# Optimization experiments

Measured on AMD Instinct MI355X. Metric: run time of the kernel, lower is better.

The kernel has to match this reference:

```python
import jax, jax.numpy as jnp
import numpy as np

H = 128          # hidden_dim
L = 3            # n_layers
G = 128          # num graphs in batch
BN_EPS = 1e-5


def setup_inputs() -> dict:
    key = jax.random.key(0)
    ks = jax.random.split(key, 16)
    N, E, ND, ED = 2048, 8192, 32, 16
    s = lambda k, shape, fan: jax.random.normal(k, shape, dtype=jnp.float32) / np.sqrt(fan)
    return {
        "x": jax.random.normal(ks[0], (N, ND), dtype=jnp.float32),
        "edge_index": jax.random.randint(ks[1], (2, E), 0, N),
        "edge_attr": jax.random.normal(ks[2], (E, ED), dtype=jnp.float32),
        "batch": jnp.sort(jax.random.randint(ks[3], (N,), 0, G)),
        "node_W": s(ks[4], (ND, H), ND),
        "node_b": jnp.zeros((H,), jnp.float32),
        "edge_W": s(ks[5], (L, ED, H * H), ED),
        "edge_b": jnp.zeros((L, H * H), jnp.float32),
        "root_W": s(ks[6], (L, H, H), H),
        "conv_bias": jnp.zeros((L, H), jnp.float32),
        "bn_gamma": jnp.ones((L, H), jnp.float32),
        "bn_beta": jnp.zeros((L, H), jnp.float32),
        "cls_W1": s(ks[7], (H, 64), H),
        "cls_b1": jnp.zeros((64,), jnp.float32),
        "cls_W2": s(ks[8], (64, 1), 64),
        "cls_b2": jnp.zeros((1,), jnp.float32),
    }


def _segment_mean(vals, ids, num_segments):
    ssum = jax.ops.segment_sum(vals, ids, num_segments=num_segments)
    cnt = jax.ops.segment_sum(jnp.ones((vals.shape[0],), vals.dtype), ids,
                              num_segments=num_segments)
    return ssum / jnp.maximum(cnt, 1.0)[:, None]


def reference(x, edge_index, edge_attr, batch, node_W, node_b, edge_W, edge_b,
              root_W, conv_bias, bn_gamma, bn_beta, cls_W1, cls_b1, cls_W2, cls_b2):
    N = x.shape[0]
    src, dst = edge_index[0], edge_index[1]
    h = x @ node_W + node_b                                   # [N, H]
    for l in range(L):
        # edge-conditioned weights: [E, H, H]
        W = (edge_attr @ edge_W[l] + edge_b[l]).reshape(-1, H, H)
        msg = jnp.einsum('ei,eio->eo', h[src], W)             # gather + per-edge matmul
        agg = _segment_mean(msg, dst, N)                      # scatter-mean
        x_new = h @ root_W[l] + agg + conv_bias[l]
        # BatchNorm (batch statistics, training-mode math)
        mu = jnp.mean(x_new, axis=0)
        var = jnp.var(x_new, axis=0)
        x_new = (x_new - mu) * jax.lax.rsqrt(var + BN_EPS) * bn_gamma[l] + bn_beta[l]
        x_new = jax.nn.relu(x_new)                            # dropout omitted (eval)
        h = h + x_new                                         # residual
    g = _segment_mean(h, batch, G)                            # global mean pool [G, H]
    out = jax.nn.relu(g @ cls_W1 + cls_b1) @ cls_W2 + cls_b2  # classifier
    return out.squeeze(-1)                                    # [G]
```

## Files before the change

kernel.cpp:

```cpp
#include <hip/hip_runtime.h>
#include <cstddef>
#include <cstdint>

#define H 128
#define EDIM 16
#define NLAYER 3
#define NSLICE 18
#define WCOLS (NSLICE * H)
#define PCOLS (EDIM * H)
#define TM 64
#define TN 64
#define TK 16

typedef unsigned short ushort_t;
typedef unsigned int uint_t;
typedef __attribute__((ext_vector_type(8))) short bf16x8;
typedef __attribute__((ext_vector_type(4))) float f32x4;

__device__ __forceinline__ ushort_t f2bf(float f) {
    uint_t u = __builtin_bit_cast(uint_t, f);
    u += 0x7fffu + ((u >> 16) & 1u);
    return (ushort_t)(u >> 16);
}
__device__ __forceinline__ float bf_lo(uint_t u) {
    return __builtin_bit_cast(float, u << 16);
}
__device__ __forceinline__ float bf_hi(uint_t u) {
    return __builtin_bit_cast(float, u & 0xffff0000u);
}

__global__ __launch_bounds__(256) void setup_kernel(
    const int* __restrict__ dst, const int* __restrict__ batch,
    int* __restrict__ hist, float* __restrict__ cntG, int E, int N,
    const float* __restrict__ eW, const float* __restrict__ eb,
    const float* __restrict__ rW, ushort_t* __restrict__ Wt)
{
    if (blockIdx.x < 32) {
        int t = blockIdx.x * 256 + threadIdx.x;
        if (t < E) atomicAdd(&hist[dst[t]], 1);
        if (t < N) atomicAdd(&cntG[batch[t]], 1.f);
        return;
    }
    __shared__ ushort_t tile[128][136];
    const int b = blockIdx.x - 32;
    const int l = b / NSLICE, s = b % NSLICE;
    const float* S = (s < 16) ? (eW + ((size_t)l * 16 + s) * (H * H))
                   : (s == 16 ? (eb + (size_t)l * H * H)
                              : (rW + (size_t)l * H * H));
    const int t = threadIdx.x;
    const int k = t >> 1, o0 = (t & 1) * 64;
#pragma unroll
    for (int j = 0; j < 64; j += 4) {
        float4 v = *(const float4*)&S[(size_t)k * H + o0 + j];
        tile[k][o0 + j + 0] = f2bf(v.x);
        tile[k][o0 + j + 1] = f2bf(v.y);
        tile[k][o0 + j + 2] = f2bf(v.z);
        tile[k][o0 + j + 3] = f2bf(v.w);
    }
    __syncthreads();
    const int n = t >> 1, k0 = (t & 1) * 64;
    ushort_t* outp = Wt + ((size_t)l * WCOLS + s * H + n) * H + k0;
#pragma unroll 8
    for (int j = 0; j < 64; ++j) outp[j] = tile[k0 + j][n];
}

__global__ __launch_bounds__(256) void scan_kernel(
    const int* __restrict__ hist, int* __restrict__ offs, int N)
{
    __shared__ int part[256];
    const int t = threadIdx.x;
    const int base = t * 8;
    int v[8], loc[8], s = 0;
#pragma unroll
    for (int j = 0; j < 8; ++j) v[j] = hist[base + j];
#pragma unroll
    for (int j = 0; j < 8; ++j) { loc[j] = s; s += v[j]; }
    part[t] = s;
    __syncthreads();
    for (int off = 1; off < 256; off <<= 1) {
        int x = (t >= off) ? part[t - off] : 0;
        __syncthreads();
        part[t] += x;
        __syncthreads();
    }
    const int boff = (t == 0) ? 0 : part[t - 1];
#pragma unroll
    for (int j = 0; j < 8; ++j) offs[base + j] = boff + loc[j];
    if (t == 255) offs[N] = boff + s;
}

__global__ void scatter_kernel(const int* __restrict__ dst,
                               const int* __restrict__ offs,
                               int* __restrict__ fill, int* __restrict__ eord, int E)
{
    const int e = blockIdx.x * 256 + threadIdx.x;
    if (e >= E) return;
    const int d = dst[e];
    const int pos = offs[d] + atomicAdd(&fill[d], 1);
    eord[pos] = e;
}

__global__ __launch_bounds__(256) void gemm_embed(
    const float* __restrict__ A, const float* __restrict__ B,
    const float* __restrict__ bias, float* __restrict__ C,
    ushort_t* __restrict__ Cbf, int M, int K, int N)
{
    __shared__ float As[TK][TM + 4];
    __shared__ float Bs[TK][TN + 4];
    const int bm = blockIdx.y * TM;
    const int bn = blockIdx.x * TN;
    const int tid = threadIdx.x;
    const int tx = tid & 15;
    const int ty = tid >> 4;

    float acc[4][4];
#pragma unroll
    for (int i = 0; i < 4; ++i)
#pragma unroll
        for (int j = 0; j < 4; ++j) acc[i][j] = 0.f;

    const int ka = tid & 15, ma = tid >> 4;
    const int nb = tid & 63, kb = tid >> 6;

    for (int k0 = 0; k0 < K; k0 += TK) {
#pragma unroll
        for (int r = 0; r < 4; ++r)
            As[ka][ma + 16 * r] = A[(size_t)(bm + ma + 16 * r) * K + (k0 + ka)];
#pragma unroll
        for (int r = 0; r < 4; ++r)
            Bs[kb + 4 * r][nb] = B[(size_t)(k0 + kb + 4 * r) * N + bn + nb];
        __syncthreads();
#pragma unroll
        for (int kk = 0; kk < TK; ++kk) {
            const float4 a4 = *(const float4*)&As[kk][ty * 4];
            const float4 b4 = *(const float4*)&Bs[kk][tx * 4];
            const float a[4] = {a4.x, a4.y, a4.z, a4.w};
            const float b[4] = {b4.x, b4.y, b4.z, b4.w};
#pragma unroll
            for (int i = 0; i < 4; ++i)
#pragma unroll
                for (int j = 0; j < 4; ++j)
                    acc[i][j] = fmaf(a[i], b[j], acc[i][j]);
        }
        __syncthreads();
    }

#pragma unroll
    for (int i = 0; i < 4; ++i) {
        const int row = bm + ty * 4 + i;
        float4 v;
        v.x = acc[i][0] + bias[(bn + tx * 4 + 0) & 127];
        v.y = acc[i][1] + bias[(bn + tx * 4 + 1) & 127];
        v.z = acc[i][2] + bias[(bn + tx * 4 + 2) & 127];
        v.w = acc[i][3] + bias[(bn + tx * 4 + 3) & 127];
        *(float4*)&C[(size_t)row * N + bn + tx * 4] = v;
        ushort_t* o = &Cbf[(size_t)row * N + bn + tx * 4];
        o[0] = f2bf(v.x); o[1] = f2bf(v.y); o[2] = f2bf(v.z); o[3] = f2bf(v.w);
    }
}

__global__ __launch_bounds__(256) void mfma_gemm(
    const ushort_t* __restrict__ hbf, const ushort_t* __restrict__ Wt,
    ushort_t* __restrict__ Pb, float* __restrict__ QR)
{
    __shared__ ushort_t As[64][136];
    __shared__ ushort_t Bs[64][136];
    const int tid = threadIdx.x;
    const int v0 = blockIdx.y * 64;
    const int n0 = blockIdx.x * 64;

    {
        const int row = tid >> 2, col0 = (tid & 3) * 32;
        const ushort_t* ga = hbf + (size_t)(v0 + row) * H + col0;
        const ushort_t* gb = Wt + (size_t)(n0 + row) * H + col0;
#pragma unroll
        for (int j = 0; j < 32; j += 8) {
            *(uint4*)&As[row][col0 + j] = *(const uint4*)(ga + j);
            *(uint4*)&Bs[row][col0 + j] = *(const uint4*)(gb + j);
        }
    }
    __syncthreads();

    const int wave = tid >> 6, lane = tid & 63;
    const int l15 = lane & 15, kg = lane >> 4;
    const int mrow = wave * 16 + l15;

    f32x4 acc0 = {0.f, 0.f, 0.f, 0.f};
    f32x4 acc1 = {0.f, 0.f, 0.f, 0.f};
    f32x4 acc2 = {0.f, 0.f, 0.f, 0.f};
    f32x4 acc3 = {0.f, 0.f, 0.f, 0.f};

#pragma unroll
    for (int s = 0; s < 4; ++s) {
        const int k = s * 32 + kg * 8;
        bf16x8 a = *(const bf16x8*)&As[mrow][k];
        bf16x8 b0 = *(const bf16x8*)&Bs[0 * 16 + l15][k];
        bf16x8 b1 = *(const bf16x8*)&Bs[1 * 16 + l15][k];
        bf16x8 b2 = *(const bf16x8*)&Bs[2 * 16 + l15][k];
        bf16x8 b3 = *(const bf16x8*)&Bs[3 * 16 + l15][k];
        acc0 = __builtin_amdgcn_mfma_f32_16x16x32_bf16(a, b0, acc0, 0, 0, 0);
        acc1 = __builtin_amdgcn_mfma_f32_16x16x32_bf16(a, b1, acc1, 0, 0, 0);
        acc2 = __builtin_amdgcn_mfma_f32_16x16x32_bf16(a, b2, acc2, 0, 0, 0);
        acc3 = __builtin_amdgcn_mfma_f32_16x16x32_bf16(a, b3, acc3, 0, 0, 0);
    }

    const int slice = n0 >> 7;
    const int lo = n0 & 127;
    const int row0 = v0 + wave * 16 + kg * 4;
    if (slice < 16) {
        ushort_t* op = Pb + (size_t)row0 * PCOLS + slice * H + lo + l15;
#pragma unroll
        for (int r = 0; r < 4; ++r) {
            op[(size_t)r * PCOLS + 0]  = f2bf(acc0[r]);
            op[(size_t)r * PCOLS + 16] = f2bf(acc1[r]);
            op[(size_t)r * PCOLS + 32] = f2bf(acc2[r]);
            op[(size_t)r * PCOLS + 48] = f2bf(acc3[r]);
        }
    } else {
        float* op = QR + (size_t)row0 * 256 + (slice - 16) * H + lo + l15;
#pragma unroll
        for (int r = 0; r < 4; ++r) {
            op[(size_t)r * 256 + 0]  = acc0[r];
            op[(size_t)r * 256 + 16] = acc1[r];
            op[(size_t)r * 256 + 32] = acc2[r];
            op[(size_t)r * 256 + 48] = acc3[r];
        }
    }
}

__global__ __launch_bounds__(256) void edge_stats(
    const ushort_t* __restrict__ Pb, const float* __restrict__ QR,
    const float* __restrict__ ea, const int* __restrict__ srcArr,
    const int* __restrict__ offs, const int* __restrict__ hist,
    const int* __restrict__ eord, const float* __restrict__ conv_b,
    float* __restrict__ xnew, float* __restrict__ bnS, float* __restrict__ bnQ)
{
    __shared__ float sS[4][H];
    __shared__ float sQ[4][H];
    const int tid = threadIdx.x;
    const int sb = tid >> 6;
    const int o2 = tid & 63;
    const int v = blockIdx.x * 4 + sb;

    const int st = offs[v];
    const int deg = hist[v];
    float m0 = 0.f, m1 = 0.f;
    for (int k = 0; k < deg; ++k) {
        const int e = eord[st + k];
        const int s = srcArr[e];
        const float* eap = ea + (size_t)e * EDIM;
        const float4 w0 = *(const float4*)(eap + 0);
        const float4 w1 = *(const float4*)(eap + 4);
        const float4 w2 = *(const float4*)(eap + 8);
        const float4 w3 = *(const float4*)(eap + 12);
        const float w[16] = {w0.x, w0.y, w0.z, w0.w, w1.x, w1.y, w1.z, w1.w,
                             w2.x, w2.y, w2.z, w2.w, w3.x, w3.y, w3.z, w3.w};
        const uint_t* prow = (const uint_t*)(Pb + (size_t)s * PCOLS) + o2;
        const float2 q2 = *(const float2*)(QR + (size_t)s * 256 + 2 * o2);
        m0 += q2.x;
        m1 += q2.y;
#pragma unroll
        for (int d = 0; d < EDIM; ++d) {
            const uint_t u = prow[(size_t)d * 64];
            m0 = fmaf(w[d], bf_lo(u), m0);
            m1 = fmaf(w[d], bf_hi(u), m1);
        }
    }
    const float rc = 1.0f / (float)(deg > 0 ? deg : 1);
    const float2 rt = *(const float2*)(QR + (size_t)v * 256 + H + 2 * o2);
    const float2 cb = *(const float2*)(conv_b + 2 * o2);
    const float val0 = m0 * rc + rt.x + cb.x;
    const float val1 = m1 * rc + rt.y + cb.y;
    *(float2*)(xnew + (size_t)v * H + 2 * o2) = make_float2(val0, val1);
    sS[sb][2 * o2] = val0; sS[sb][2 * o2 + 1] = val1;
    sQ[sb][2 * o2] = val0 * val0; sQ[sb][2 * o2 + 1] = val1 * val1;
    __syncthreads();
    if (tid < H) {
        const float s4 = sS[0][tid] + sS[1][tid] + sS[2][tid] + sS[3][tid];
        const float q4 = sQ[0][tid] + sQ[1][tid] + sQ[2][tid] + sQ[3][tid];
        atomicAdd(&bnS[tid], s4);
        atomicAdd(&bnQ[tid], q4);
    }
}

__global__ __launch_bounds__(256) void bn_apply(
    float* __restrict__ h, ushort_t* __restrict__ hbf,
    const float* __restrict__ xnew,
    const float* __restrict__ bnS, const float* __restrict__ bnQ,
    const float* __restrict__ gamma, const float* __restrict__ beta,
    const int* __restrict__ batch, float* __restrict__ gsum, int N, int last)
{
    const int idx = blockIdx.x * 256 + threadIdx.x;
    const int c = idx & 127;
    const int v = idx >> 7;
    const float invN = 1.0f / (float)N;
    const float mu = bnS[c] * invN;
    const float var = bnQ[c] * invN - mu * mu;
    const float val = (xnew[idx] - mu) * rsqrtf(var + 1e-5f) * gamma[c] + beta[c];
    const float hn = h[idx] + fmaxf(val, 0.f);
    h[idx] = hn;
    hbf[idx] = f2bf(hn);
    if (last) atomicAdd(&gsum[batch[v] * H + c], hn);
}

__global__ void classifier_kernel(
    const float* __restrict__ gsum, const float* __restrict__ cntG,
    const float* __restrict__ W1, const float* __restrict__ b1,
    const float* __restrict__ W2, const float* __restrict__ b2,
    float* __restrict__ out)
{
    const int g = blockIdx.x;
    const int j = threadIdx.x;
    const float rc = 1.0f / fmaxf(cntG[g], 1.0f);
    float acc = b1[j];
#pragma unroll 8
    for (int i = 0; i < H; ++i)
        acc = fmaf(gsum[g * H + i] * rc, W1[i * 64 + j], acc);
    float pv = fmaxf(acc, 0.f) * W2[j];
#pragma unroll
    for (int off = 32; off > 0; off >>= 1)
        pv += __shfl_down(pv, off);
    if (j == 0) out[g] = pv + b2[0];
}

extern "C" void kernel_launch(void* const* d_in, const int* in_sizes, int n_in,
                              void* d_out, int out_size, void* d_ws, size_t ws_size,
                              hipStream_t stream)
{
    const float* x      = (const float*)d_in[0];
    const int*   eidx   = (const int*)  d_in[1];
    const float* eattr  = (const float*)d_in[2];
    const int*   batch  = (const int*)  d_in[3];
    const float* node_W = (const float*)d_in[4];
    const float* node_b = (const float*)d_in[5];
    const float* edge_W = (const float*)d_in[6];
    const float* edge_b = (const float*)d_in[7];
    const float* root_W = (const float*)d_in[8];
    const float* conv_b = (const float*)d_in[9];
    const float* gamma  = (const float*)d_in[10];
    const float* beta   = (const float*)d_in[11];
    const float* W1     = (const float*)d_in[12];
    const float* b1     = (const float*)d_in[13];
    const float* W2     = (const float*)d_in[14];
    const float* b2     = (const float*)d_in[15];
    float* out = (float*)d_out;

    const int N = in_sizes[0] / 32;
    const int E = in_sizes[1] / 2;
    const int G = out_size;

    int* hist   = (int*)d_ws;
    int* fill   = hist + N;
    float* cntG = (float*)(fill + N);
    float* bnS  = cntG + G;
    float* bnQ  = bnS + NLAYER * H;
    float* gsum = bnQ + NLAYER * H;
    int* offs   = (int*)(gsum + (size_t)G * H);
    int* eord   = offs + (N + 16);
    float* h    = (float*)(eord + E);
    float* xnew = h + (size_t)N * H;
    ushort_t* hbf = (ushort_t*)(xnew + (size_t)N * H);
    ushort_t* Wt  = hbf + (size_t)N * H;
    ushort_t* Pb  = Wt + (size_t)NLAYER * WCOLS * H;
    float* QR   = (float*)(Pb + (size_t)N * PCOLS);

    const size_t zbytes = (size_t)(2 * N) * 4
                        + ((size_t)G + 2 * NLAYER * H + (size_t)G * H) * 4;
    hipMemsetAsync(hist, 0, zbytes, stream);

    const int* src = eidx;
    const int* dst = eidx + E;

    setup_kernel<<<32 + NLAYER * NSLICE, 256, 0, stream>>>(
        dst, batch, hist, cntG, E, N, edge_W, edge_b, root_W, Wt);
    scan_kernel<<<1, 256, 0, stream>>>(hist, offs, N);
    scatter_kernel<<<E / 256, 256, 0, stream>>>(dst, offs, fill, eord, E);

    gemm_embed<<<dim3(H / TN, N / TM), 256, 0, stream>>>(
        x, node_W, node_b, h, hbf, N, 32, H);

    for (int l = 0; l < NLAYER; ++l) {
        mfma_gemm<<<dim3(WCOLS / 64, N / 64), 256, 0, stream>>>(
            hbf, Wt + (size_t)l * WCOLS * H, Pb, QR);
        edge_stats<<<N / 4, 256, 0, stream>>>(
            Pb, QR, eattr, src, offs, hist, eord,
            conv_b + (size_t)l * H, xnew, bnS + l * H, bnQ + l * H);
        bn_apply<<<(N * H) / 256, 256, 0, stream>>>(
            h, hbf, xnew, bnS + l * H, bnQ + l * H,
            gamma + (size_t)l * H, beta + (size_t)l * H,
            batch, gsum, N, l == NLAYER - 1);
    }

    classifier_kernel<<<G, 64, 0, stream>>>(gsum, cntG, W1, b1, W2, b2, out);
}
```

Baseline: 206.2 us.

## Replace CSR gather aggregation with per-edge atomic scatter and merge setup kernels

Drops the scan and scatter kernels that built a destination-sorted edge order. Each edge is now handled by one wave that computes its message and atomically adds it into a zeroed fp32 aggregation buffer, and a separate node_stats kernel applies mean normalisation, root and bias terms, BN statistics and re-zeroes the buffer. The node embedding GEMM is folded into the setup kernel as extra blocks. This cuts kernel launches and avoids degree-imbalanced per-node loops, at the cost of many fp32 atomics, an extra kernel per layer, and nondeterministic summation order.

```diff
diff --git a/kernel.cpp b/kernel.cpp
--- a/kernel.cpp
+++ b/kernel.cpp
@@ -8,9 +8,6 @@
 #define NSLICE 18
 #define WCOLS (NSLICE * H)
 #define PCOLS (EDIM * H)
-#define TM 64
-#define TN 64
-#define TK 16
 
 typedef unsigned short ushort_t;
 typedef unsigned int uint_t;
@@ -31,107 +28,72 @@
 
 __global__ __launch_bounds__(256) void setup_kernel(
     const int* __restrict__ dst, const int* __restrict__ batch,
-    int* __restrict__ hist, float* __restrict__ cntG, int E, int N,
+    int* __restrict__ histD, float* __restrict__ cntG, int E, int N,
     const float* __restrict__ eW, const float* __restrict__ eb,
-    const float* __restrict__ rW, ushort_t* __restrict__ Wt)
-{
+    const float* __restrict__ rW, ushort_t* __restrict__ Wt,
+    const float* __restrict__ x, const float* __restrict__ nW,
+    const float* __restrict__ nbias, float* __restrict__ h,
+    ushort_t* __restrict__ hbf)
+{
+    __shared__ alignas(16) ushort_t tile[128][136];
+    const int t = threadIdx.x;
+
     if (blockIdx.x < 32) {
-        int t = blockIdx.x * 256 + threadIdx.x;
-        if (t < E) atomicAdd(&hist[dst[t]], 1);
-        if (t < N) atomicAdd(&cntG[batch[t]], 1.f);
+        const int g = blockIdx.x * 256 + t;
+        if (g < E) atomicAdd(&histD[dst[g]], 1);
+        if (g < N) atomicAdd(&cntG[batch[g]], 1.f);
         return;
     }
-    __shared__ ushort_t tile[128][136];
-    const int b = blockIdx.x - 32;
-    const int l = b / NSLICE, s = b % NSLICE;
-    const float* S = (s < 16) ? (eW + ((size_t)l * 16 + s) * (H * H))
-                   : (s == 16 ? (eb + (size_t)l * H * H)
-                              : (rW + (size_t)l * H * H));
-    const int t = threadIdx.x;
-    const int k = t >> 1, o0 = (t & 1) * 64;
-#pragma unroll
-    for (int j = 0; j < 64; j += 4) {
-        float4 v = *(const float4*)&S[(size_t)k * H + o0 + j];
-        tile[k][o0 + j + 0] = f2bf(v.x);
-        tile[k][o0 + j + 1] = f2bf(v.y);
-        tile[k][o0 + j + 2] = f2bf(v.z);
-        tile[k][o0 + j + 3] = f2bf(v.w);
-    }
-    __syncthreads();
-    const int n = t >> 1, k0 = (t & 1) * 64;
-    ushort_t* outp = Wt + ((size_t)l * WCOLS + s * H + n) * H + k0;
+
+    if (blockIdx.x < 86) {
+        const int b = blockIdx.x - 32;
+        const int l = b / NSLICE, s = b % NSLICE;
+        const float* S = (s < 16) ? (eW + ((size_t)l * 16 + s) * (H * H))
+                       : (s == 16 ? (eb + (size_t)l * H * H)
+                                  : (rW + (size_t)l * H * H));
+        const int k = t >> 1, o0 = (t & 1) * 64;
+#pragma unroll
+        for (int j = 0; j < 64; j += 4) {
+            float4 v = *(const float4*)&S[(size_t)k * H + o0 + j];
+            tile[k][o0 + j + 0] = f2bf(v.x);
+            tile[k][o0 + j + 1] = f2bf(v.y);
+            tile[k][o0 + j + 2] = f2bf(v.z);
+            tile[k][o0 + j + 3] = f2bf(v.w);
+        }
+        __syncthreads();
+        const int n = t >> 1, k0 = (t & 1) * 64;
+        ushort_t* outp = Wt + ((size_t)l * WCOLS + s * H + n) * H + k0;
 #pragma unroll 8
-    for (int j = 0; j < 64; ++j) outp[j] = tile[k0 + j][n];
-}
-
-__global__ __launch_bounds__(256) void scan_kernel(
-    const int* __restrict__ hist, int* __restrict__ offs, int N)
-{
-    __shared__ int part[256];
-    const int t = threadIdx.x;
-    const int base = t * 8;
-    int v[8], loc[8], s = 0;
-#pragma unroll
-    for (int j = 0; j < 8; ++j) v[j] = hist[base + j];
-#pragma unroll
-    for (int j = 0; j < 8; ++j) { loc[j] = s; s += v[j]; }
-    part[t] = s;
-    __syncthreads();
-    for (int off = 1; off < 256; off <<= 1) {
-        int x = (t >= off) ? part[t - off] : 0;
+        for (int j = 0; j < 64; ++j) outp[j] = tile[k0 + j][n];
+        return;
+    }
+
+    const int b2 = blockIdx.x - 86;
+    const int bm = (b2 >> 1) * 64;
+    const int bn = (b2 & 1) * 64;
+    float (*As)[68] = (float (*)[68])(void*)tile;
+    float (*Bs)[68] = ((float (*)[68])(void*)tile) + 16;
+
+    const int tx = t & 15, ty = t >> 4;
+    float acc[4][4];
+#pragma unroll
+    for (int i = 0; i < 4; ++i)
+#pragma unroll
+        for (int j = 0; j < 4; ++j) acc[i][j] = 0.f;
+
+    const int ka = t & 15, ma = t >> 4;
+    const int nb2 = t & 63, kb = t >> 6;
+
+    for (int k0 = 0; k0 < 32; k0 += 16) {
+#pragma unroll
+        for (int r = 0; r < 4; ++r)
+            As[ka][ma + 16 * r] = x[(size_t)(bm + ma + 16 * r) * 32 + k0 + ka];
+#pragma unroll
+        for (int r = 0; r < 4; ++r)
+            Bs[kb + 4 * r][nb2] = nW[(size_t)(k0 + kb + 4 * r) * H + bn + nb2];
         __syncthreads();
-        part[t] += x;
-        __syncthreads();
-    }
-    const int boff = (t == 0) ? 0 : part[t - 1];
-#pragma unroll
-    for (int j = 0; j < 8; ++j) offs[base + j] = boff + loc[j];
-    if (t == 255) offs[N] = boff + s;
-}
-
-__global__ void scatter_kernel(const int* __restrict__ dst,
-                               const int* __restrict__ offs,
-                               int* __restrict__ fill, int* __restrict__ eord, int E)
-{
-    const int e = blockIdx.x * 256 + threadIdx.x;
-    if (e >= E) return;
-    const int d = dst[e];
-    const int pos = offs[d] + atomicAdd(&fill[d], 1);
-    eord[pos] = e;
-}
-
-__global__ __launch_bounds__(256) void gemm_embed(
-    const float* __restrict__ A, const float* __restrict__ B,
-    const float* __restrict__ bias, float* __restrict__ C,
-    ushort_t* __restrict__ Cbf, int M, int K, int N)
-{
-    __shared__ float As[TK][TM + 4];
-    __shared__ float Bs[TK][TN + 4];
-    const int bm = blockIdx.y * TM;
-    const int bn = blockIdx.x * TN;
-    const int tid = threadIdx.x;
-    const int tx = tid & 15;
-    const int ty = tid >> 4;
-
-    float acc[4][4];
-#pragma unroll
-    for (int i = 0; i < 4; ++i)
-#pragma unroll
-        for (int j = 0; j < 4; ++j) acc[i][j] = 0.f;
-
-    const int ka = tid & 15, ma = tid >> 4;
-    const int nb = tid & 63, kb = tid >> 6;
-
-    for (int k0 = 0; k0 < K; k0 += TK) {
-#pragma unroll
-        for (int r = 0; r < 4; ++r)
-            As[ka][ma + 16 * r] = A[(size_t)(bm + ma + 16 * r) * K + (k0 + ka)];
-#pragma unroll
-        for (int r = 0; r < 4; ++r)
-            Bs[kb + 4 * r][nb] = B[(size_t)(k0 + kb + 4 * r) * N + bn + nb];
-        __syncthreads();
-#pragma unroll
-        for (int kk = 0; kk < TK; ++kk) {
+#pragma unroll
+        for (int kk = 0; kk < 16; ++kk) {
             const float4 a4 = *(const float4*)&As[kk][ty * 4];
             const float4 b4 = *(const float4*)&Bs[kk][tx * 4];
             const float a[4] = {a4.x, a4.y, a4.z, a4.w};
@@ -149,12 +111,12 @@
     for (int i = 0; i < 4; ++i) {
         const int row = bm + ty * 4 + i;
         float4 v;
-        v.x = acc[i][0] + bias[(bn + tx * 4 + 0) & 127];
-        v.y = acc[i][1] + bias[(bn + tx * 4 + 1) & 127];
-        v.z = acc[i][2] + bias[(bn + tx * 4 + 2) & 127];
-        v.w = acc[i][3] + bias[(bn + tx * 4 + 3) & 127];
-        *(float4*)&C[(size_t)row * N + bn + tx * 4] = v;
-        ushort_t* o = &Cbf[(size_t)row * N + bn + tx * 4];
+        v.x = acc[i][0] + nbias[bn + tx * 4 + 0];
+        v.y = acc[i][1] + nbias[bn + tx * 4 + 1];
+        v.z = acc[i][2] + nbias[bn + tx * 4 + 2];
+        v.w = acc[i][3] + nbias[bn + tx * 4 + 3];
+        *(float4*)&h[(size_t)row * H + bn + tx * 4] = v;
+        ushort_t* o = &hbf[(size_t)row * H + bn + tx * 4];
         o[0] = f2bf(v.x); o[1] = f2bf(v.y); o[2] = f2bf(v.z); o[3] = f2bf(v.w);
     }
 }
@@ -228,58 +190,65 @@
     }
 }
 
-__global__ __launch_bounds__(256) void edge_stats(
+__global__ __launch_bounds__(256) void edge_msg(
     const ushort_t* __restrict__ Pb, const float* __restrict__ QR,
     const float* __restrict__ ea, const int* __restrict__ srcArr,
-    const int* __restrict__ offs, const int* __restrict__ hist,
-    const int* __restrict__ eord, const float* __restrict__ conv_b,
+    const int* __restrict__ dstArr, float* __restrict__ agg, int E)
+{
+    const int wave = threadIdx.x >> 6, lane = threadIdx.x & 63;
+    const int e = blockIdx.x * 4 + wave;
+    if (e >= E) return;
+    const int s  = srcArr[e];
+    const int dv = dstArr[e];
+    const float* eap = ea + (size_t)e * EDIM;
+    const float4 w0 = *(const float4*)(eap + 0);
+    const float4 w1 = *(const float4*)(eap + 4);
+    const float4 w2 = *(const float4*)(eap + 8);
+    const float4 w3 = *(const float4*)(eap + 12);
+    const float w[16] = {w0.x, w0.y, w0.z, w0.w, w1.x, w1.y, w1.z, w1.w,
+                         w2.x, w2.y, w2.z, w2.w, w3.x, w3.y, w3.z, w3.w};
+    const uint_t* prow = (const uint_t*)Pb + (size_t)s * (PCOLS / 2) + lane;
+    const float2 q2 = *(const float2*)(QR + (size_t)s * 256 + 2 * lane);
+    float m0 = q2.x, m1 = q2.y;
+#pragma unroll
+    for (int d = 0; d < EDIM; ++d) {
+        const uint_t u = prow[(size_t)d * 64];
+        m0 = fmaf(w[d], bf_lo(u), m0);
+        m1 = fmaf(w[d], bf_hi(u), m1);
+    }
+    atomicAdd(&agg[(size_t)dv * H + 2 * lane], m0);
+    atomicAdd(&agg[(size_t)dv * H + 2 * lane + 1], m1);
+}
+
+__global__ __launch_bounds__(256) void node_stats(
+    float* __restrict__ agg, const float* __restrict__ QR,
+    const int* __restrict__ histD, const float* __restrict__ conv_b,
     float* __restrict__ xnew, float* __restrict__ bnS, float* __restrict__ bnQ)
 {
-    __shared__ float sS[4][H];
-    __shared__ float sQ[4][H];
+    __shared__ float sS[H];
+    __shared__ float sQ[H];
     const int tid = threadIdx.x;
-    const int sb = tid >> 6;
-    const int o2 = tid & 63;
-    const int v = blockIdx.x * 4 + sb;
-
-    const int st = offs[v];
-    const int deg = hist[v];
-    float m0 = 0.f, m1 = 0.f;
-    for (int k = 0; k < deg; ++k) {
-        const int e = eord[st + k];
-        const int s = srcArr[e];
-        const float* eap = ea + (size_t)e * EDIM;
-        const float4 w0 = *(const float4*)(eap + 0);
-        const float4 w1 = *(const float4*)(eap + 4);
-        const float4 w2 = *(const float4*)(eap + 8);
-        const float4 w3 = *(const float4*)(eap + 12);
-        const float w[16] = {w0.x, w0.y, w0.z, w0.w, w1.x, w1.y, w1.z, w1.w,
-                             w2.x, w2.y, w2.z, w2.w, w3.x, w3.y, w3.z, w3.w};
-        const uint_t* prow = (const uint_t*)(Pb + (size_t)s * PCOLS) + o2;
-        const float2 q2 = *(const float2*)(QR + (size_t)s * 256 + 2 * o2);
-        m0 += q2.x;
-        m1 += q2.y;
-#pragma unroll
-        for (int d = 0; d < EDIM; ++d) {
-            const uint_t u = prow[(size_t)d * 64];
-            m0 = fmaf(w[d], bf_lo(u), m0);
-            m1 = fmaf(w[d], bf_hi(u), m1);
-        }
-    }
-    const float rc = 1.0f / (float)(deg > 0 ? deg : 1);
-    const float2 rt = *(const float2*)(QR + (size_t)v * 256 + H + 2 * o2);
-    const float2 cb = *(const float2*)(conv_b + 2 * o2);
-    const float val0 = m0 * rc + rt.x + cb.x;
-    const float val1 = m1 * rc + rt.y + cb.y;
-    *(float2*)(xnew + (size_t)v * H + 2 * o2) = make_float2(val0, val1);
-    sS[sb][2 * o2] = val0; sS[sb][2 * o2 + 1] = val1;
-    sQ[sb][2 * o2] = val0 * val0; sQ[sb][2 * o2 + 1] = val1 * val1;
+    const int c = tid & 127, half = tid >> 7;
+    const int v0 = blockIdx.x * 8 + half * 4;
+    const float cb = conv_b[c];
+    float s = 0.f, q = 0.f;
+#pragma unroll
+    for (int j = 0; j < 4; ++j) {
+        const int v = v0 + j;
+        const int deg = histD[v];
+        const float rc = 1.0f / (float)(deg > 0 ? deg : 1);
+        const size_t ix = (size_t)v * H + c;
+        const float val = agg[ix] * rc + QR[(size_t)v * 256 + H + c] + cb;
+        xnew[ix] = val;
+        agg[ix] = 0.f;
+        s += val;
+        q += val * val;
+    }
+    if (half == 0) { sS[c] = s; sQ[c] = q; }
     __syncthreads();
-    if (tid < H) {
-        const float s4 = sS[0][tid] + sS[1][tid] + sS[2][tid] + sS[3][tid];
-        const float q4 = sQ[0][tid] + sQ[1][tid] + sQ[2][tid] + sQ[3][tid];
-        atomicAdd(&bnS[tid], s4);
-        atomicAdd(&bnQ[tid], q4);
+    if (half == 1) {
+        atomicAdd(&bnS[c], sS[c] + s);
+        atomicAdd(&bnQ[c], sQ[c] + q);
     }
 }
 
@@ -349,42 +318,38 @@
     const int E = in_sizes[1] / 2;
     const int G = out_size;
 
-    int* hist   = (int*)d_ws;
-    int* fill   = hist + N;
-    float* cntG = (float*)(fill + N);
+    int* histD  = (int*)d_ws;
+    float* cntG = (float*)(histD + N);
     float* bnS  = cntG + G;
     float* bnQ  = bnS + NLAYER * H;
     float* gsum = bnQ + NLAYER * H;
-    int* offs   = (int*)(gsum + (size_t)G * H);
-    int* eord   = offs + (N + 16);
-    float* h    = (float*)(eord + E);
+    float* agg  = gsum + (size_t)G * H;
+    float* h    = agg + (size_t)N * H;
     float* xnew = h + (size_t)N * H;
     ushort_t* hbf = (ushort_t*)(xnew + (size_t)N * H);
     ushort_t* Wt  = hbf + (size_t)N * H;
     ushort_t* Pb  = Wt + (size_t)NLAYER * WCOLS * H;
     float* QR   = (float*)(Pb + (size_t)N * PCOLS);
 
-    const size_t zbytes = (size_t)(2 * N) * 4
-                        + ((size_t)G + 2 * NLAYER * H + (size_t)G * H) * 4;
-    hipMemsetAsync(hist, 0, zbytes, stream);
+    const size_t zbytes = ((size_t)N + G + 2 * NLAYER * H
+                         + (size_t)G * H + (size_t)N * H) * 4;
+    hipMemsetAsync(d_ws, 0, zbytes, stream);
 
     const int* src = eidx;
     const int* dst = eidx + E;
 
-    setup_kernel<<<32 + NLAYER * NSLICE, 256, 0, stream>>>(
-        dst, batch, hist, cntG, E, N, edge_W, edge_b, root_W, Wt);
-    scan_kernel<<<1, 256, 0, stream>>>(hist, offs, N);
-    scatter_kernel<<<E / 256, 256, 0, stream>>>(dst, offs, fill, eord, E);
-
-    gemm_embed<<<dim3(H / TN, N / TM), 256, 0, stream>>>(
-        x, node_W, node_b, h, hbf, N, 32, H);
+    setup_kernel<<<150, 256, 0, stream>>>(
+        dst, batch, histD, cntG, E, N, edge_W, edge_b, root_W, Wt,
+        x, node_W, node_b, h, hbf);
 
     for (int l = 0; l < NLAYER; ++l) {
         mfma_gemm<<<dim3(WCOLS / 64, N / 64), 256, 0, stream>>>(
             hbf, Wt + (size_t)l * WCOLS * H, Pb, QR);
-        edge_stats<<<N / 4, 256, 0, stream>>>(
-            Pb, QR, eattr, src, offs, hist, eord,
-            conv_b + (size_t)l * H, xnew, bnS + l * H, bnQ + l * H);
+        edge_msg<<<(E + 3) / 4, 256, 0, stream>>>(
+            Pb, QR, eattr, src, dst, agg, E);
+        node_stats<<<N / 8, 256, 0, stream>>>(
+            agg, QR, histD, conv_b + (size_t)l * H,
+            xnew, bnS + l * H, bnQ + l * H);
         bn_apply<<<(N * H) / 256, 256, 0, stream>>>(
             h, hbf, xnew, bnS + l * H, bnQ + l * H,
             gamma + (size_t)l * H, beta + (size_t)l * H,
```

After: 198.9 us. 1.04x faster.
